# Kernel optimization log

Hardware: AMD Instinct MI355X
Metric: run time of the kernel (lower is better)

The kernel has to match this reference:

```python
import jax, jax.numpy as jnp
import numpy as np

B, H, HKV, SQ, SKV, D = 2, 16, 4, 2048, 2048, 64
G = H // HKV  # query heads per kv head group
NSEG = 8


def setup_inputs() -> dict:
    key = jax.random.key(0)
    kq, kk, kv_, ks1, ks2 = jax.random.split(key, 5)
    q = jax.random.normal(kq, (B, H, SQ, D), dtype=jnp.float32)
    k = jax.random.normal(kk, (B, HKV, SKV, D), dtype=jnp.float32)
    v = jax.random.normal(kv_, (B, HKV, SKV, D), dtype=jnp.float32)
    q_segment_ids = jnp.sort(jax.random.randint(ks1, (B, SQ), 0, NSEG, dtype=jnp.int32), axis=-1)
    kv_segment_ids = jnp.sort(jax.random.randint(ks2, (B, SKV), 0, NSEG, dtype=jnp.int32), axis=-1)
    return {"q": q, "k": k, "v": v, "q_segment_ids": q_segment_ids, "kv_segment_ids": kv_segment_ids}


def reference(q, k, v, q_segment_ids, kv_segment_ids):
    # q: [B,H,SQ,D], k/v: [B,HKV,SKV,D]; GQA: each kv head serves G query heads.
    softmax_scale = 1.0 / jnp.sqrt(jnp.asarray(D, jnp.float32))
    qg = q.reshape(B, HKV, G, SQ, D)
    # scores: [B,HKV,G,SQ,SKV]
    scores = jnp.einsum("bhgsd,bhtd->bhgst", qg, k) * softmax_scale
    # segment mask: attend only within the same segment, and q_seg must be >= 0
    same_seg = (q_segment_ids[:, :, None] == kv_segment_ids[:, None, :]) & (
        q_segment_ids[:, :, None] >= 0
    )  # [B,SQ,SKV]
    mask = same_seg[:, None, None, :, :]
    masked_scores = jnp.where(mask, scores, -jnp.inf)
    m = jnp.max(masked_scores, axis=-1)  # [B,HKV,G,SQ], may be -inf for fully-masked rows
    m_safe = jnp.where(m == -jnp.inf, 0.0, m)
    p = jnp.where(mask, jnp.exp(scores - m_safe[..., None]), 0.0)
    l = jnp.sum(p, axis=-1)  # [B,HKV,G,SQ]
    acc = jnp.einsum("bhgst,bhtd->bhgsd", p, v)
    l_safe = jnp.where(l == 0.0, 1.0, l)
    out = jnp.where((l == 0.0)[..., None], 0.0, acc / l_safe[..., None])
    return out.reshape(B, H, SQ, D)
```

## Files before the change

### kernel.cpp

```cpp
#include <hip/hip_runtime.h>
#include <hip/hip_bf16.h>

#define NB   2
#define NH   16
#define NHKV 4
#define GQ   4
#define SQL  2048
#define SKV  2048
#define DH   64
#define QBLK 64
#define KVBLK 64
#define LDK  72

#define QSCALE (0.125f * 1.44269504f)
#define M2REF  (4.0f * 1.44269504f)

typedef __bf16 v8bf  __attribute__((ext_vector_type(8)));
typedef float  f32x4 __attribute__((ext_vector_type(4)));

__global__ __launch_bounds__(256, 3)
void gqa_seg_attn(const float* __restrict__ q,
                  const float* __restrict__ k,
                  const float* __restrict__ v,
                  const int* __restrict__ qseg,
                  const int* __restrict__ kvseg,
                  float* __restrict__ out)
{
    __shared__ __bf16 k_lds[2][KVBLK][LDK];
    __shared__ __bf16 vT_lds[2][DH][LDK];
    __shared__ __bf16 p_lds[4][16][LDK];

    const int tid  = threadIdx.x;
    const int lane = tid & 63;
    const int w    = tid >> 6;
    const int qt   = blockIdx.x;
    const int h    = blockIdx.y;
    const int b    = blockIdx.z;
    const int kvh  = h / GQ;
    const int q0   = qt * QBLK;

    const float* qptr  = q + (((size_t)b * NH   + h  ) * SQL) * DH;
    const float* kptr  = k + (((size_t)b * NHKV + kvh) * SKV) * DH;
    const float* vptr  = v + (((size_t)b * NHKV + kvh) * SKV) * DH;
    const int*   qsegb = qseg  + (size_t)b * SQL;
    const int*   kvsegb= kvseg + (size_t)b * SKV;

    const int l15 = lane & 15;
    const int lg  = lane >> 4;
    const int d_a = lg * 8;

    v8bf qfrag[2];
    {
        const int qrow = q0 + w * 16 + l15;
        for (int c = 0; c < 2; ++c) {
            const float* src = qptr + (size_t)qrow * DH + c * 32 + d_a;
            float4 f0 = *(const float4*)(src);
            float4 f1 = *(const float4*)(src + 4);
            v8bf t;
            t[0] = (__bf16)(f0.x * QSCALE); t[1] = (__bf16)(f0.y * QSCALE);
            t[2] = (__bf16)(f0.z * QSCALE); t[3] = (__bf16)(f0.w * QSCALE);
            t[4] = (__bf16)(f1.x * QSCALE); t[5] = (__bf16)(f1.y * QSCALE);
            t[6] = (__bf16)(f1.z * QSCALE); t[7] = (__bf16)(f1.w * QSCALE);
            qfrag[c] = t;
        }
    }

    const int qrow_c0 = q0 + w * 16 + (lg << 2);
    int qsegr[4];
    for (int r = 0; r < 4; ++r) qsegr[r] = qsegb[qrow_c0 + r];

    const int wsmin = qsegb[q0 + w * 16];
    const int wsmax = qsegb[q0 + w * 16 + 15];

    const int smin = qsegb[q0];
    const int smax = qsegb[q0 + QBLK - 1];
    int lo, hi;
    {
        int a = 0, e = SKV;
        while (a < e) { int m = (a + e) >> 1; if (kvsegb[m] <  smin) a = m + 1; else e = m; }
        lo = a;
        a = lo; e = SKV;
        while (a < e) { int m = (a + e) >> 1; if (kvsegb[m] <= smax) a = m + 1; else e = m; }
        hi = a;
    }
    int t0i = lo >> 6;
    int t1i = (hi + KVBLK - 1) >> 6;
    if (hi <= lo) t1i = t0i;
    const int nt = t1i - t0i;

    const int krow = tid >> 2, kc0 = (tid & 3) * 16;
    const int vcol = tid & 63, vd0 = (tid >> 6) * 16;

    float4 ka[4], va[4];
    int kvs_cur[4], kvs_nxt[4];

    auto issue = [&](int kt) {
        const int kv0 = kt * KVBLK;
        for (int r2 = 0; r2 < 4; ++r2)
            kvs_nxt[r2] = kvsegb[kv0 + r2 * 16 + l15];
        const float* ks = kptr + (size_t)(kv0 + krow) * DH + kc0;
        const float* vs = vptr + (size_t)(kv0 + vcol) * DH + vd0;
        for (int i2 = 0; i2 < 4; ++i2) {
            ka[i2] = *(const float4*)(ks + 4 * i2);
            va[i2] = *(const float4*)(vs + 4 * i2);
        }
    };
    auto commit = [&](int p) {
        v8bf ta, tb;
        ta[0] = (__bf16)ka[0].x; ta[1] = (__bf16)ka[0].y;
        ta[2] = (__bf16)ka[0].z; ta[3] = (__bf16)ka[0].w;
        ta[4] = (__bf16)ka[1].x; ta[5] = (__bf16)ka[1].y;
        ta[6] = (__bf16)ka[1].z; ta[7] = (__bf16)ka[1].w;
        tb[0] = (__bf16)ka[2].x; tb[1] = (__bf16)ka[2].y;
        tb[2] = (__bf16)ka[2].z; tb[3] = (__bf16)ka[2].w;
        tb[4] = (__bf16)ka[3].x; tb[5] = (__bf16)ka[3].y;
        tb[6] = (__bf16)ka[3].z; tb[7] = (__bf16)ka[3].w;
        *(v8bf*)&k_lds[p][krow][kc0]     = ta;
        *(v8bf*)&k_lds[p][krow][kc0 + 8] = tb;
        for (int i2 = 0; i2 < 4; ++i2) {
            vT_lds[p][vd0 + 4 * i2 + 0][vcol] = (__bf16)va[i2].x;
            vT_lds[p][vd0 + 4 * i2 + 1][vcol] = (__bf16)va[i2].y;
            vT_lds[p][vd0 + 4 * i2 + 2][vcol] = (__bf16)va[i2].z;
            vT_lds[p][vd0 + 4 * i2 + 3][vcol] = (__bf16)va[i2].w;
        }
        for (int r2 = 0; r2 < 4; ++r2) kvs_cur[r2] = kvs_nxt[r2];
    };

    float l_acc[4];
    f32x4 o_acc[4];
    for (int r = 0; r < 4; ++r) l_acc[r] = 0.f;
    for (int t = 0; t < 4; ++t) o_acc[t] = (f32x4){0.f, 0.f, 0.f, 0.f};

    if (nt > 0) { issue(t0i); commit(0); }

    for (int i = 0; i < nt; ++i) {
        __syncthreads();
        const int p = i & 1;
        if (i + 1 < nt) issue(t0i + i + 1);

        const int tmin = __shfl(kvs_cur[0], 0);
        const int tmax = __shfl(kvs_cur[3], 15);
        if (!(tmax < wsmin || tmin > wsmax)) {
            f32x4 s[4];
            for (int n = 0; n < 4; ++n) s[n] = (f32x4){0.f, 0.f, 0.f, 0.f};
            for (int n = 0; n < 4; ++n)
                for (int c = 0; c < 2; ++c) {
                    v8bf kb = *(const v8bf*)&k_lds[p][n * 16 + l15][c * 32 + d_a];
                    s[n] = __builtin_amdgcn_mfma_f32_16x16x32_bf16(qfrag[c], kb, s[n], 0, 0, 0);
                }
            for (int n = 0; n < 4; ++n)
                for (int r = 0; r < 4; ++r) {
                    float sv = (kvs_cur[n] == qsegr[r]) ? s[n][r] : -__builtin_inff();
                    float pv = __builtin_amdgcn_exp2f(sv - M2REF);
                    l_acc[r] += pv;
                    p_lds[w][(lg << 2) + r][n * 16 + l15] = (__bf16)pv;
                }
            v8bf pa[2];
            for (int c = 0; c < 2; ++c)
                pa[c] = *(const v8bf*)&p_lds[w][l15][c * 32 + d_a];
            for (int t = 0; t < 4; ++t)
                for (int c = 0; c < 2; ++c) {
                    v8bf vb = *(const v8bf*)&vT_lds[p][t * 16 + l15][c * 32 + d_a];
                    o_acc[t] = __builtin_amdgcn_mfma_f32_16x16x32_bf16(pa[c], vb, o_acc[t], 0, 0, 0);
                }
        }

        if (i + 1 < nt) commit((i + 1) & 1);
    }

    float* outp = out + (((size_t)b * NH + h) * SQL) * DH;
    for (int r = 0; r < 4; ++r) {
        float x = l_acc[r];
        for (int d = 1; d < 16; d <<= 1) x += __shfl_xor(x, d);
        float inv = (x > 0.f) ? (1.f / x) : 0.f;
        for (int t = 0; t < 4; ++t)
            outp[(size_t)(qrow_c0 + r) * DH + t * 16 + l15] = o_acc[t][r] * inv;
    }
}

extern "C" void kernel_launch(void* const* d_in, const int* in_sizes, int n_in,
                              void* d_out, int out_size, void* d_ws, size_t ws_size,
                              hipStream_t stream) {
    const float* q     = (const float*)d_in[0];
    const float* k     = (const float*)d_in[1];
    const float* v     = (const float*)d_in[2];
    const int*   qseg  = (const int*)d_in[3];
    const int*   kvseg = (const int*)d_in[4];
    float* out = (float*)d_out;

    dim3 grid(SQL / QBLK, NH, NB);
    dim3 block(256);
    gqa_seg_attn<<<grid, block, 0, stream>>>(q, k, v, qseg, kvseg, out);
}
```

Before: 41.08 us.

## Use persistent blocks with an atomic work queue and MFMA priority hints

Replaces the fixed 3D grid with a persistent grid of 768 blocks. Each block pulls (q-tile, head, batch) tasks from a global atomic counter in the workspace, which is reset by a small extra kernel launched before it. This is meant to balance the uneven per-tile work that segment skipping creates. It also raises wave priority around the MFMA sections with s_setprio. The cost is one extra kernel launch, atomics and extra barriers per task, and a loss of the natural ordering of tiles.

```diff
diff --git a/kernel.cpp b/kernel.cpp
--- a/kernel.cpp
+++ b/kernel.cpp
@@ -11,12 +11,16 @@
 #define QBLK 64
 #define KVBLK 64
 #define LDK  72
+#define NTASK (32 * NH * NB)
+#define GRID  768
 
 #define QSCALE (0.125f * 1.44269504f)
 #define M2REF  (4.0f * 1.44269504f)
 
 typedef __bf16 v8bf  __attribute__((ext_vector_type(8)));
 typedef float  f32x4 __attribute__((ext_vector_type(4)));
+
+__global__ void init_counter(unsigned* cnt) { if (threadIdx.x == 0) *cnt = 0u; }
 
 __global__ __launch_bounds__(256, 3)
 void gqa_seg_attn(const float* __restrict__ q,
@@ -24,157 +28,174 @@
                   const float* __restrict__ v,
                   const int* __restrict__ qseg,
                   const int* __restrict__ kvseg,
-                  float* __restrict__ out)
+                  float* __restrict__ out,
+                  unsigned* __restrict__ cnt)
 {
     __shared__ __bf16 k_lds[2][KVBLK][LDK];
     __shared__ __bf16 vT_lds[2][DH][LDK];
     __shared__ __bf16 p_lds[4][16][LDK];
+    __shared__ int    task_s;
 
     const int tid  = threadIdx.x;
     const int lane = tid & 63;
     const int w    = tid >> 6;
-    const int qt   = blockIdx.x;
-    const int h    = blockIdx.y;
-    const int b    = blockIdx.z;
-    const int kvh  = h / GQ;
-    const int q0   = qt * QBLK;
-
-    const float* qptr  = q + (((size_t)b * NH   + h  ) * SQL) * DH;
-    const float* kptr  = k + (((size_t)b * NHKV + kvh) * SKV) * DH;
-    const float* vptr  = v + (((size_t)b * NHKV + kvh) * SKV) * DH;
-    const int*   qsegb = qseg  + (size_t)b * SQL;
-    const int*   kvsegb= kvseg + (size_t)b * SKV;
-
-    const int l15 = lane & 15;
-    const int lg  = lane >> 4;
-    const int d_a = lg * 8;
-
-    v8bf qfrag[2];
-    {
-        const int qrow = q0 + w * 16 + l15;
-        for (int c = 0; c < 2; ++c) {
-            const float* src = qptr + (size_t)qrow * DH + c * 32 + d_a;
-            float4 f0 = *(const float4*)(src);
-            float4 f1 = *(const float4*)(src + 4);
-            v8bf t;
-            t[0] = (__bf16)(f0.x * QSCALE); t[1] = (__bf16)(f0.y * QSCALE);
-            t[2] = (__bf16)(f0.z * QSCALE); t[3] = (__bf16)(f0.w * QSCALE);
-            t[4] = (__bf16)(f1.x * QSCALE); t[5] = (__bf16)(f1.y * QSCALE);
-            t[6] = (__bf16)(f1.z * QSCALE); t[7] = (__bf16)(f1.w * QSCALE);
-            qfrag[c] = t;
-        }
-    }
-
-    const int qrow_c0 = q0 + w * 16 + (lg << 2);
-    int qsegr[4];
-    for (int r = 0; r < 4; ++r) qsegr[r] = qsegb[qrow_c0 + r];
-
-    const int wsmin = qsegb[q0 + w * 16];
-    const int wsmax = qsegb[q0 + w * 16 + 15];
-
-    const int smin = qsegb[q0];
-    const int smax = qsegb[q0 + QBLK - 1];
-    int lo, hi;
-    {
-        int a = 0, e = SKV;
-        while (a < e) { int m = (a + e) >> 1; if (kvsegb[m] <  smin) a = m + 1; else e = m; }
-        lo = a;
-        a = lo; e = SKV;
-        while (a < e) { int m = (a + e) >> 1; if (kvsegb[m] <= smax) a = m + 1; else e = m; }
-        hi = a;
-    }
-    int t0i = lo >> 6;
-    int t1i = (hi + KVBLK - 1) >> 6;
-    if (hi <= lo) t1i = t0i;
-    const int nt = t1i - t0i;
+    const int l15  = lane & 15;
+    const int lg   = lane >> 4;
+    const int d_a  = lg * 8;
 
     const int krow = tid >> 2, kc0 = (tid & 3) * 16;
     const int vcol = tid & 63, vd0 = (tid >> 6) * 16;
 
-    float4 ka[4], va[4];
-    int kvs_cur[4], kvs_nxt[4];
-
-    auto issue = [&](int kt) {
-        const int kv0 = kt * KVBLK;
-        for (int r2 = 0; r2 < 4; ++r2)
-            kvs_nxt[r2] = kvsegb[kv0 + r2 * 16 + l15];
-        const float* ks = kptr + (size_t)(kv0 + krow) * DH + kc0;
-        const float* vs = vptr + (size_t)(kv0 + vcol) * DH + vd0;
-        for (int i2 = 0; i2 < 4; ++i2) {
-            ka[i2] = *(const float4*)(ks + 4 * i2);
-            va[i2] = *(const float4*)(vs + 4 * i2);
-        }
-    };
-    auto commit = [&](int p) {
-        v8bf ta, tb;
-        ta[0] = (__bf16)ka[0].x; ta[1] = (__bf16)ka[0].y;
-        ta[2] = (__bf16)ka[0].z; ta[3] = (__bf16)ka[0].w;
-        ta[4] = (__bf16)ka[1].x; ta[5] = (__bf16)ka[1].y;
-        ta[6] = (__bf16)ka[1].z; ta[7] = (__bf16)ka[1].w;
-        tb[0] = (__bf16)ka[2].x; tb[1] = (__bf16)ka[2].y;
-        tb[2] = (__bf16)ka[2].z; tb[3] = (__bf16)ka[2].w;
-        tb[4] = (__bf16)ka[3].x; tb[5] = (__bf16)ka[3].y;
-        tb[6] = (__bf16)ka[3].z; tb[7] = (__bf16)ka[3].w;
-        *(v8bf*)&k_lds[p][krow][kc0]     = ta;
-        *(v8bf*)&k_lds[p][krow][kc0 + 8] = tb;
-        for (int i2 = 0; i2 < 4; ++i2) {
-            vT_lds[p][vd0 + 4 * i2 + 0][vcol] = (__bf16)va[i2].x;
-            vT_lds[p][vd0 + 4 * i2 + 1][vcol] = (__bf16)va[i2].y;
-            vT_lds[p][vd0 + 4 * i2 + 2][vcol] = (__bf16)va[i2].z;
-            vT_lds[p][vd0 + 4 * i2 + 3][vcol] = (__bf16)va[i2].w;
-        }
-        for (int r2 = 0; r2 < 4; ++r2) kvs_cur[r2] = kvs_nxt[r2];
-    };
-
-    float l_acc[4];
-    f32x4 o_acc[4];
-    for (int r = 0; r < 4; ++r) l_acc[r] = 0.f;
-    for (int t = 0; t < 4; ++t) o_acc[t] = (f32x4){0.f, 0.f, 0.f, 0.f};
-
-    if (nt > 0) { issue(t0i); commit(0); }
-
-    for (int i = 0; i < nt; ++i) {
+    for (;;) {
+        if (tid == 0) task_s = atomicAdd(cnt, 1u);
         __syncthreads();
-        const int p = i & 1;
-        if (i + 1 < nt) issue(t0i + i + 1);
-
-        const int tmin = __shfl(kvs_cur[0], 0);
-        const int tmax = __shfl(kvs_cur[3], 15);
-        if (!(tmax < wsmin || tmin > wsmax)) {
-            f32x4 s[4];
-            for (int n = 0; n < 4; ++n) s[n] = (f32x4){0.f, 0.f, 0.f, 0.f};
-            for (int n = 0; n < 4; ++n)
-                for (int c = 0; c < 2; ++c) {
-                    v8bf kb = *(const v8bf*)&k_lds[p][n * 16 + l15][c * 32 + d_a];
-                    s[n] = __builtin_amdgcn_mfma_f32_16x16x32_bf16(qfrag[c], kb, s[n], 0, 0, 0);
+        const int task = task_s;
+        __syncthreads();
+        if (task >= NTASK) break;
+
+        const int qt = task & 31;
+        const int h  = (task >> 5) & 15;
+        const int b  = task >> 9;
+        const int kvh = h / GQ;
+        const int q0  = qt * QBLK;
+
+        const float* qptr   = q + (((size_t)b * NH   + h  ) * SQL) * DH;
+        const float* kptr   = k + (((size_t)b * NHKV + kvh) * SKV) * DH;
+        const float* vptr   = v + (((size_t)b * NHKV + kvh) * SKV) * DH;
+        const int*   qsegb  = qseg  + (size_t)b * SQL;
+        const int*   kvsegb = kvseg + (size_t)b * SKV;
+
+        v8bf qfrag[2];
+        {
+            const int qrow = q0 + w * 16 + l15;
+            for (int c = 0; c < 2; ++c) {
+                const float* src = qptr + (size_t)qrow * DH + c * 32 + d_a;
+                float4 f0 = *(const float4*)(src);
+                float4 f1 = *(const float4*)(src + 4);
+                v8bf t;
+                t[0] = (__bf16)(f0.x * QSCALE); t[1] = (__bf16)(f0.y * QSCALE);
+                t[2] = (__bf16)(f0.z * QSCALE); t[3] = (__bf16)(f0.w * QSCALE);
+                t[4] = (__bf16)(f1.x * QSCALE); t[5] = (__bf16)(f1.y * QSCALE);
+                t[6] = (__bf16)(f1.z * QSCALE); t[7] = (__bf16)(f1.w * QSCALE);
+                qfrag[c] = t;
+            }
+        }
+
+        const int qrow_c0 = q0 + w * 16 + (lg << 2);
+        int qsegr[4];
+        for (int r = 0; r < 4; ++r) qsegr[r] = qsegb[qrow_c0 + r];
+
+        const int wsmin = qsegb[q0 + w * 16];
+        const int wsmax = qsegb[q0 + w * 16 + 15];
+
+        const int smin = qsegb[q0];
+        const int smax = qsegb[q0 + QBLK - 1];
+        int lo, hi;
+        {
+            int a = 0, e = SKV;
+            while (a < e) { int m = (a + e) >> 1; if (kvsegb[m] <  smin) a = m + 1; else e = m; }
+            lo = a;
+            a = lo; e = SKV;
+            while (a < e) { int m = (a + e) >> 1; if (kvsegb[m] <= smax) a = m + 1; else e = m; }
+            hi = a;
+        }
+        int t0i = lo >> 6;
+        int t1i = (hi + KVBLK - 1) >> 6;
+        if (hi <= lo) t1i = t0i;
+        const int nt = t1i - t0i;
+
+        float4 ka[4], va[4];
+        int kvs_cur[4], kvs_nxt[4];
+
+        auto issue = [&](int kt) {
+            const int kv0 = kt * KVBLK;
+            for (int r2 = 0; r2 < 4; ++r2)
+                kvs_nxt[r2] = kvsegb[kv0 + r2 * 16 + l15];
+            const float* ks = kptr + (size_t)(kv0 + krow) * DH + kc0;
+            const float* vs = vptr + (size_t)(kv0 + vcol) * DH + vd0;
+            for (int i2 = 0; i2 < 4; ++i2) {
+                ka[i2] = *(const float4*)(ks + 4 * i2);
+                va[i2] = *(const float4*)(vs + 4 * i2);
+            }
+        };
+        auto commit = [&](int p) {
+            v8bf ta, tb;
+            ta[0] = (__bf16)ka[0].x; ta[1] = (__bf16)ka[0].y;
+            ta[2] = (__bf16)ka[0].z; ta[3] = (__bf16)ka[0].w;
+            ta[4] = (__bf16)ka[1].x; ta[5] = (__bf16)ka[1].y;
+            ta[6] = (__bf16)ka[1].z; ta[7] = (__bf16)ka[1].w;
+            tb[0] = (__bf16)ka[2].x; tb[1] = (__bf16)ka[2].y;
+            tb[2] = (__bf16)ka[2].z; tb[3] = (__bf16)ka[2].w;
+            tb[4] = (__bf16)ka[3].x; tb[5] = (__bf16)ka[3].y;
+            tb[6] = (__bf16)ka[3].z; tb[7] = (__bf16)ka[3].w;
+            *(v8bf*)&k_lds[p][krow][kc0]     = ta;
+            *(v8bf*)&k_lds[p][krow][kc0 + 8] = tb;
+            for (int i2 = 0; i2 < 4; ++i2) {
+                vT_lds[p][vd0 + 4 * i2 + 0][vcol] = (__bf16)va[i2].x;
+                vT_lds[p][vd0 + 4 * i2 + 1][vcol] = (__bf16)va[i2].y;
+                vT_lds[p][vd0 + 4 * i2 + 2][vcol] = (__bf16)va[i2].z;
+                vT_lds[p][vd0 + 4 * i2 + 3][vcol] = (__bf16)va[i2].w;
+            }
+            for (int r2 = 0; r2 < 4; ++r2) kvs_cur[r2] = kvs_nxt[r2];
+        };
+
+        float l_acc[4];
+        f32x4 o_acc[4];
+        for (int r = 0; r < 4; ++r) l_acc[r] = 0.f;
+        for (int t = 0; t < 4; ++t) o_acc[t] = (f32x4){0.f, 0.f, 0.f, 0.f};
+
+        if (nt > 0) { issue(t0i); commit(0); }
+
+        for (int i = 0; i < nt; ++i) {
+            __syncthreads();
+            const int p = i & 1;
+            if (i + 1 < nt) issue(t0i + i + 1);
+
+            const int tmin = __shfl(kvs_cur[0], 0);
+            const int tmax = __shfl(kvs_cur[3], 15);
+            if (!(tmax < wsmin || tmin > wsmax)) {
+                f32x4 s[4];
+                __builtin_amdgcn_s_setprio(1);
+                for (int n = 0; n < 4; ++n) {
+                    s[n] = (f32x4){0.f, 0.f, 0.f, 0.f};
+                    for (int c = 0; c < 2; ++c) {
+                        v8bf kb = *(const v8bf*)&k_lds[p][n * 16 + l15][c * 32 + d_a];
+                        s[n] = __builtin_amdgcn_mfma_f32_16x16x32_bf16(qfrag[c], kb, s[n], 0, 0, 0);
+                    }
                 }
-            for (int n = 0; n < 4; ++n)
-                for (int r = 0; r < 4; ++r) {
-                    float sv = (kvs_cur[n] == qsegr[r]) ? s[n][r] : -__builtin_inff();
-                    float pv = __builtin_amdgcn_exp2f(sv - M2REF);
-                    l_acc[r] += pv;
-                    p_lds[w][(lg << 2) + r][n * 16 + l15] = (__bf16)pv;
-                }
-            v8bf pa[2];
-            for (int c = 0; c < 2; ++c)
-                pa[c] = *(const v8bf*)&p_lds[w][l15][c * 32 + d_a];
+                __builtin_amdgcn_s_setprio(0);
+                for (int n = 0; n < 4; ++n)
+                    for (int r = 0; r < 4; ++r) {
+                        float sv = (kvs_cur[n] == qsegr[r]) ? s[n][r] : -__builtin_inff();
+                        float pv = __builtin_amdgcn_exp2f(sv - M2REF);
+                        l_acc[r] += pv;
+                        p_lds[w][(lg << 2) + r][n * 16 + l15] = (__bf16)pv;
+                    }
+                v8bf pa[2];
+                for (int c = 0; c < 2; ++c)
+                    pa[c] = *(const v8bf*)&p_lds[w][l15][c * 32 + d_a];
+                __builtin_amdgcn_s_setprio(1);
+                for (int t = 0; t < 4; ++t)
+                    for (int c = 0; c < 2; ++c) {
+                        v8bf vb = *(const v8bf*)&vT_lds[p][t * 16 + l15][c * 32 + d_a];
+                        o_acc[t] = __builtin_amdgcn_mfma_f32_16x16x32_bf16(pa[c], vb, o_acc[t], 0, 0, 0);
+                    }
+                __builtin_amdgcn_s_setprio(0);
+            }
+
+            if (i + 1 < nt) commit((i + 1) & 1);
+        }
+
+        float* outp = out + (((size_t)b * NH + h) * SQL) * DH;
+        for (int r = 0; r < 4; ++r) {
+            float x = l_acc[r];
+            for (int d = 1; d < 16; d <<= 1) x += __shfl_xor(x, d);
+            float inv = (x > 0.f) ? (1.f / x) : 0.f;
             for (int t = 0; t < 4; ++t)
-                for (int c = 0; c < 2; ++c) {
-                    v8bf vb = *(const v8bf*)&vT_lds[p][t * 16 + l15][c * 32 + d_a];
-                    o_acc[t] = __builtin_amdgcn_mfma_f32_16x16x32_bf16(pa[c], vb, o_acc[t], 0, 0, 0);
-                }
-        }
-
-        if (i + 1 < nt) commit((i + 1) & 1);
-    }
-
-    float* outp = out + (((size_t)b * NH + h) * SQL) * DH;
-    for (int r = 0; r < 4; ++r) {
-        float x = l_acc[r];
-        for (int d = 1; d < 16; d <<= 1) x += __shfl_xor(x, d);
-        float inv = (x > 0.f) ? (1.f / x) : 0.f;
-        for (int t = 0; t < 4; ++t)
-            outp[(size_t)(qrow_c0 + r) * DH + t * 16 + l15] = o_acc[t][r] * inv;
+                outp[(size_t)(qrow_c0 + r) * DH + t * 16 + l15] = o_acc[t][r] * inv;
+        }
+
+        __syncthreads();
     }
 }
 
@@ -187,8 +208,8 @@
     const int*   qseg  = (const int*)d_in[3];
     const int*   kvseg = (const int*)d_in[4];
     float* out = (float*)d_out;
-
-    dim3 grid(SQL / QBLK, NH, NB);
-    dim3 block(256);
-    gqa_seg_attn<<<grid, block, 0, stream>>>(q, k, v, qseg, kvseg, out);
+    unsigned* cnt = (unsigned*)d_ws;
+
+    init_counter<<<dim3(1), dim3(64), 0, stream>>>(cnt);
+    gqa_seg_attn<<<dim3(GRID), dim3(256), 0, stream>>>(q, k, v, qseg, kvseg, out, cnt);
 }
```

After: 55.46 us. +35.0%, slower.

## Load K fragments directly from global, drop K LDS staging, raise occupancy

Applied to the files above, without the earlier changes.

Removes the K shared-memory double buffer: each wave now reads its K MFMA operands straight from global memory and converts them to bf16 in registers, and only for tiles whose segments overlap the wave. V staging is re-mapped so each thread writes packed bf16 pairs into the transposed V buffer, replacing scalar writes. The softmax reference offset is folded into the MFMA accumulator initialisation, s_setprio is wrapped around the MFMA sections, and launch bounds are raised to allow more resident blocks. The goal is to cut LDS traffic and footprint, at the cost of synchronous global loads on the critical path without prefetch, and K is re-read by each of the four waves.

```diff
diff --git a/kernel.cpp b/kernel.cpp
--- a/kernel.cpp
+++ b/kernel.cpp
@@ -16,9 +16,17 @@
 #define M2REF  (4.0f * 1.44269504f)
 
 typedef __bf16 v8bf  __attribute__((ext_vector_type(8)));
+typedef __bf16 v2bf  __attribute__((ext_vector_type(2)));
 typedef float  f32x4 __attribute__((ext_vector_type(4)));
 
-__global__ __launch_bounds__(256, 3)
+__device__ __forceinline__ v8bf cvtbf8(float4 a, float4 b) {
+  v8bf t;
+  t[0]=(__bf16)a.x; t[1]=(__bf16)a.y; t[2]=(__bf16)a.z; t[3]=(__bf16)a.w;
+  t[4]=(__bf16)b.x; t[5]=(__bf16)b.y; t[6]=(__bf16)b.z; t[7]=(__bf16)b.w;
+  return t;
+}
+
+__global__ __launch_bounds__(256, 5)
 void gqa_seg_attn(const float* __restrict__ q,
                   const float* __restrict__ k,
                   const float* __restrict__ v,
@@ -26,7 +34,6 @@
                   const int* __restrict__ kvseg,
                   float* __restrict__ out)
 {
-    __shared__ __bf16 k_lds[2][KVBLK][LDK];
     __shared__ __bf16 vT_lds[2][DH][LDK];
     __shared__ __bf16 p_lds[4][16][LDK];
 
@@ -39,11 +46,11 @@
     const int kvh  = h / GQ;
     const int q0   = qt * QBLK;
 
-    const float* qptr  = q + (((size_t)b * NH   + h  ) * SQL) * DH;
-    const float* kptr  = k + (((size_t)b * NHKV + kvh) * SKV) * DH;
-    const float* vptr  = v + (((size_t)b * NHKV + kvh) * SKV) * DH;
-    const int*   qsegb = qseg  + (size_t)b * SQL;
-    const int*   kvsegb= kvseg + (size_t)b * SKV;
+    const float* qptr   = q + (((size_t)b * NH   + h  ) * SQL) * DH;
+    const float* kptr   = k + (((size_t)b * NHKV + kvh) * SKV) * DH;
+    const float* vptr   = v + (((size_t)b * NHKV + kvh) * SKV) * DH;
+    const int*   qsegb  = qseg  + (size_t)b * SQL;
+    const int*   kvsegb = kvseg + (size_t)b * SKV;
 
     const int l15 = lane & 15;
     const int lg  = lane >> 4;
@@ -88,41 +95,33 @@
     if (hi <= lo) t1i = t0i;
     const int nt = t1i - t0i;
 
-    const int krow = tid >> 2, kc0 = (tid & 3) * 16;
-    const int vcol = tid & 63, vd0 = (tid >> 6) * 16;
-
-    float4 ka[4], va[4];
+    const int kp  = tid & 31;
+    const int vd0 = (tid >> 5) * 8;
+
+    float4 va[4];
     int kvs_cur[4], kvs_nxt[4];
 
     auto issue = [&](int kt) {
         const int kv0 = kt * KVBLK;
         for (int r2 = 0; r2 < 4; ++r2)
             kvs_nxt[r2] = kvsegb[kv0 + r2 * 16 + l15];
-        const float* ks = kptr + (size_t)(kv0 + krow) * DH + kc0;
-        const float* vs = vptr + (size_t)(kv0 + vcol) * DH + vd0;
-        for (int i2 = 0; i2 < 4; ++i2) {
-            ka[i2] = *(const float4*)(ks + 4 * i2);
-            va[i2] = *(const float4*)(vs + 4 * i2);
-        }
+        const float* vs0 = vptr + (size_t)(kv0 + 2 * kp) * DH + vd0;
+        const float* vs1 = vs0 + DH;
+        va[0] = *(const float4*)(vs0);
+        va[1] = *(const float4*)(vs0 + 4);
+        va[2] = *(const float4*)(vs1);
+        va[3] = *(const float4*)(vs1 + 4);
     };
     auto commit = [&](int p) {
-        v8bf ta, tb;
-        ta[0] = (__bf16)ka[0].x; ta[1] = (__bf16)ka[0].y;
-        ta[2] = (__bf16)ka[0].z; ta[3] = (__bf16)ka[0].w;
-        ta[4] = (__bf16)ka[1].x; ta[5] = (__bf16)ka[1].y;
-        ta[6] = (__bf16)ka[1].z; ta[7] = (__bf16)ka[1].w;
-        tb[0] = (__bf16)ka[2].x; tb[1] = (__bf16)ka[2].y;
-        tb[2] = (__bf16)ka[2].z; tb[3] = (__bf16)ka[2].w;
-        tb[4] = (__bf16)ka[3].x; tb[5] = (__bf16)ka[3].y;
-        tb[6] = (__bf16)ka[3].z; tb[7] = (__bf16)ka[3].w;
-        *(v8bf*)&k_lds[p][krow][kc0]     = ta;
-        *(v8bf*)&k_lds[p][krow][kc0 + 8] = tb;
-        for (int i2 = 0; i2 < 4; ++i2) {
-            vT_lds[p][vd0 + 4 * i2 + 0][vcol] = (__bf16)va[i2].x;
-            vT_lds[p][vd0 + 4 * i2 + 1][vcol] = (__bf16)va[i2].y;
-            vT_lds[p][vd0 + 4 * i2 + 2][vcol] = (__bf16)va[i2].z;
-            vT_lds[p][vd0 + 4 * i2 + 3][vcol] = (__bf16)va[i2].w;
-        }
+        v2bf t;
+        t[0] = (__bf16)va[0].x; t[1] = (__bf16)va[2].x; *(v2bf*)&vT_lds[p][vd0+0][2*kp] = t;
+        t[0] = (__bf16)va[0].y; t[1] = (__bf16)va[2].y; *(v2bf*)&vT_lds[p][vd0+1][2*kp] = t;
+        t[0] = (__bf16)va[0].z; t[1] = (__bf16)va[2].z; *(v2bf*)&vT_lds[p][vd0+2][2*kp] = t;
+        t[0] = (__bf16)va[0].w; t[1] = (__bf16)va[2].w; *(v2bf*)&vT_lds[p][vd0+3][2*kp] = t;
+        t[0] = (__bf16)va[1].x; t[1] = (__bf16)va[3].x; *(v2bf*)&vT_lds[p][vd0+4][2*kp] = t;
+        t[0] = (__bf16)va[1].y; t[1] = (__bf16)va[3].y; *(v2bf*)&vT_lds[p][vd0+5][2*kp] = t;
+        t[0] = (__bf16)va[1].z; t[1] = (__bf16)va[3].z; *(v2bf*)&vT_lds[p][vd0+6][2*kp] = t;
+        t[0] = (__bf16)va[1].w; t[1] = (__bf16)va[3].w; *(v2bf*)&vT_lds[p][vd0+7][2*kp] = t;
         for (int r2 = 0; r2 < 4; ++r2) kvs_cur[r2] = kvs_nxt[r2];
     };
 
@@ -136,33 +135,43 @@
     for (int i = 0; i < nt; ++i) {
         __syncthreads();
         const int p = i & 1;
+        const int kv0 = (t0i + i) * KVBLK;
         if (i + 1 < nt) issue(t0i + i + 1);
 
         const int tmin = __shfl(kvs_cur[0], 0);
         const int tmax = __shfl(kvs_cur[3], 15);
         if (!(tmax < wsmin || tmin > wsmax)) {
+            v8bf kbf[4][2];
+            for (int n = 0; n < 4; ++n) {
+                const float* ks = kptr + (size_t)(kv0 + n * 16 + l15) * DH + d_a;
+                kbf[n][0] = cvtbf8(*(const float4*)(ks),      *(const float4*)(ks + 4));
+                kbf[n][1] = cvtbf8(*(const float4*)(ks + 32), *(const float4*)(ks + 36));
+            }
             f32x4 s[4];
-            for (int n = 0; n < 4; ++n) s[n] = (f32x4){0.f, 0.f, 0.f, 0.f};
-            for (int n = 0; n < 4; ++n)
-                for (int c = 0; c < 2; ++c) {
-                    v8bf kb = *(const v8bf*)&k_lds[p][n * 16 + l15][c * 32 + d_a];
-                    s[n] = __builtin_amdgcn_mfma_f32_16x16x32_bf16(qfrag[c], kb, s[n], 0, 0, 0);
-                }
+            __builtin_amdgcn_s_setprio(1);
+            for (int n = 0; n < 4; ++n) {
+                s[n] = (f32x4){-M2REF, -M2REF, -M2REF, -M2REF};
+                for (int c = 0; c < 2; ++c)
+                    s[n] = __builtin_amdgcn_mfma_f32_16x16x32_bf16(qfrag[c], kbf[n][c], s[n], 0, 0, 0);
+            }
+            __builtin_amdgcn_s_setprio(0);
             for (int n = 0; n < 4; ++n)
                 for (int r = 0; r < 4; ++r) {
                     float sv = (kvs_cur[n] == qsegr[r]) ? s[n][r] : -__builtin_inff();
-                    float pv = __builtin_amdgcn_exp2f(sv - M2REF);
+                    float pv = __builtin_amdgcn_exp2f(sv);
                     l_acc[r] += pv;
                     p_lds[w][(lg << 2) + r][n * 16 + l15] = (__bf16)pv;
                 }
             v8bf pa[2];
             for (int c = 0; c < 2; ++c)
                 pa[c] = *(const v8bf*)&p_lds[w][l15][c * 32 + d_a];
+            __builtin_amdgcn_s_setprio(1);
             for (int t = 0; t < 4; ++t)
                 for (int c = 0; c < 2; ++c) {
                     v8bf vb = *(const v8bf*)&vT_lds[p][t * 16 + l15][c * 32 + d_a];
                     o_acc[t] = __builtin_amdgcn_mfma_f32_16x16x32_bf16(pa[c], vb, o_acc[t], 0, 0, 0);
                 }
+            __builtin_amdgcn_s_setprio(0);
         }
 
         if (i + 1 < nt) commit((i + 1) & 1);
```

Result: slower. 86.48 us (+110.5%).
